# Kernel tuning notes

Measured on AMD Instinct MI355X. Metric: run time of the kernel, lower is better.

## Reference

```python
import jax, jax.numpy as jnp
import numpy as np

B, M, N, C = 8, 4096, 4096, 3


def setup_inputs() -> dict:
    key = jax.random.key(0)
    k1, k2 = jax.random.split(key)
    set1 = jax.random.normal(k1, (B, M, C), dtype=jnp.float32)
    set2 = jax.random.normal(k2, (B, N, C), dtype=jnp.float32)
    return {"set1": set1, "set2": set2}


def _pairwise_dist(set1, set2):
    # ||a - b|| computed via expansion to avoid a (B,M,N,C) broadcast tensor.
    sq1 = jnp.sum(set1 * set1, axis=-1)  # (B, M)
    sq2 = jnp.sum(set2 * set2, axis=-1)  # (B, N)
    inner = jnp.einsum("bmc,bnc->bmn", set1, set2)  # (B, M, N)
    d2 = sq1[:, :, None] + sq2[:, None, :] - 2.0 * inner
    return jnp.sqrt(jnp.maximum(d2, 0.0))  # (B, M, N)


def reference(set1, set2):
    # Average (Chamfer-style) Hausdorff: mean of directed nearest-neighbor
    # distances in both directions, summed.  Output shape (B,).
    d = _pairwise_dist(set1, set2)                # (B, M, N)
    term_1 = jnp.mean(jnp.min(d, axis=2), axis=1)  # set1 -> set2
    term_2 = jnp.mean(jnp.min(d, axis=1), axis=1)  # set2 -> set1
    res = term_1 + term_2
    if res.shape[0] == 1:
        res = jnp.squeeze(res, axis=0)
    return res
```

## Files before the change

kernel.cpp:

```cpp
#include <hip/hip_runtime.h>
#include <hip/hip_bf16.h>
#include <math.h>

constexpr int NB   = 8;
constexpr int NPTS = 4096;
constexpr int NSEG = 4;
constexpr int NN   = NPTS / NSEG;

typedef __attribute__((ext_vector_type(8)))  short  short8;
typedef __attribute__((ext_vector_type(16))) float  f32x16;

__device__ inline unsigned short f2bf(float v) {
    __hip_bfloat16 t = __float2bfloat16(v);
    return *reinterpret_cast<unsigned short*>(&t);
}
__device__ inline float bf2f(unsigned short u) {
    __hip_bfloat16 t = *reinterpret_cast<__hip_bfloat16*>(&u);
    return __bfloat162float(t);
}

__global__ __launch_bounds__(256, 4) void mfma_min_kernel(
    const float* __restrict__ s1, const float* __restrict__ s2,
    float* __restrict__ pmin)
{
    __shared__ short8 blds[2048];

    int bid  = blockIdx.x;
    int nseg = bid & 3;
    int qb   = (bid >> 2) & 15;
    int g    = bid >> 6;
    int b    = g & 7, dir = g >> 3;

    const float* Q    = dir ? s2 : s1;
    const float* Tset = dir ? s1 : s2;

    int tid = threadIdx.x;
    int wid = tid >> 6, l = tid & 63;
    int c = l & 31, h = l >> 5;

    const float* tsrc = Tset + ((size_t)b * NPTS + (size_t)nseg * NN) * 3;
    #pragma unroll
    for (int k = 0; k < 4; ++k) {
        int p = k * 256 + tid;
        float x = tsrc[p*3+0], y = tsrc[p*3+1], z = tsrc[p*3+2];
        float sq = fmaf(z, z, fmaf(y, y, x * x));
        float tx = -2.0f*x, ty = -2.0f*y, tz = -2.0f*z;
        unsigned short thx = f2bf(tx), thy = f2bf(ty), thz = f2bf(tz);
        unsigned short tlx = f2bf(tx - bf2f(thx));
        unsigned short tly = f2bf(ty - bf2f(thy));
        unsigned short tlz = f2bf(tz - bf2f(thz));
        unsigned short sqh = f2bf(sq);
        unsigned short sql = f2bf(sq - bf2f(sqh));
        short8 tLo = {(short)thx,(short)thy,(short)thz,(short)thx,(short)thy,(short)thz,(short)sqh,(short)sql};
        short8 tHi = {(short)tlx,(short)tly,(short)tlz,0,0,0,0,0};
        int slot = (p >> 5) * 64 + (p & 31);
        blds[slot]      = tLo;
        blds[slot + 32] = tHi;
    }

    short8 qfr[2];
    #pragma unroll
    for (int f = 0; f < 2; ++f) {
        int qidx = qb * 256 + wid * 64 + f * 32 + c;
        const float* qp = Q + ((size_t)b * NPTS + qidx) * 3;
        float x = qp[0], y = qp[1], z = qp[2];
        unsigned short ahx = f2bf(x), ahy = f2bf(y), ahz = f2bf(z);
        if (h == 0) {
            unsigned short alx = f2bf(x - bf2f(ahx));
            unsigned short aly = f2bf(y - bf2f(ahy));
            unsigned short alz = f2bf(z - bf2f(ahz));
            unsigned short one = 0x3F80;
            qfr[f] = short8{(short)ahx,(short)ahy,(short)ahz,
                            (short)alx,(short)aly,(short)alz,(short)one,(short)one};
        } else {
            qfr[f] = short8{(short)ahx,(short)ahy,(short)ahz,0,0,0,0,0};
        }
    }
    __syncthreads();

    f32x16 zero, acc0, acc1;
    #pragma unroll
    for (int r = 0; r < 16; ++r) { zero[r] = 0.0f; acc0[r] = 3.4e38f; acc1[r] = 3.4e38f; }

    for (int i = 0; i < 16; ++i) {
        short8 t0 = blds[(2*i  ) * 64 + l];
        short8 t1 = blds[(2*i+1) * 64 + l];
        {
            f32x16 d0 = __builtin_amdgcn_mfma_f32_32x32x16_bf16(t0, qfr[0], zero, 0, 0, 0);
            f32x16 d1 = __builtin_amdgcn_mfma_f32_32x32x16_bf16(t1, qfr[0], zero, 0, 0, 0);
            #pragma unroll
            for (int r = 0; r < 16; ++r)
                acc0[r] = fminf(fminf(acc0[r], d0[r]), d1[r]);
        }
        {
            f32x16 d0 = __builtin_amdgcn_mfma_f32_32x32x16_bf16(t0, qfr[1], zero, 0, 0, 0);
            f32x16 d1 = __builtin_amdgcn_mfma_f32_32x32x16_bf16(t1, qfr[1], zero, 0, 0, 0);
            #pragma unroll
            for (int r = 0; r < 16; ++r)
                acc1[r] = fminf(fminf(acc1[r], d0[r]), d1[r]);
        }
    }

    float* pg = pmin + ((size_t)g * NSEG + nseg) * NPTS;
    #pragma unroll
    for (int f = 0; f < 2; ++f) {
        f32x16& a = f ? acc1 : acc0;
        float v = a[0];
        #pragma unroll
        for (int r = 1; r < 16; ++r) v = fminf(v, a[r]);
        v = fminf(v, __shfl_xor(v, 32, 64));
        if (h == 0)
            pg[qb * 256 + wid * 64 + f * 32 + c] = v;
    }
}

__global__ __launch_bounds__(1024) void reduce_kernel(
    const float* __restrict__ s1, const float* __restrict__ s2,
    const float* __restrict__ pmin, float* __restrict__ out)
{
    int b = blockIdx.x;
    int t = threadIdx.x;

    float sum = 0.0f;
    #pragma unroll
    for (int dir = 0; dir < 2; ++dir) {
        int g = dir * NB + b;
        const float4* pg = reinterpret_cast<const float4*>(pmin + (size_t)g * NSEG * NPTS);
        float4 m = pg[t];
        #pragma unroll
        for (int s = 1; s < NSEG; ++s) {
            float4 v = pg[(size_t)s * 1024 + t];
            m.x = fminf(m.x, v.x); m.y = fminf(m.y, v.y);
            m.z = fminf(m.z, v.z); m.w = fminf(m.w, v.w);
        }
        const float* q = (dir ? s2 : s1) + ((size_t)b * NPTS + (size_t)4 * t) * 3;
        const float4* q4 = reinterpret_cast<const float4*>(q);
        float4 f0 = q4[0], f1 = q4[1], f2 = q4[2];
        float sa0 = fmaf(f0.z, f0.z, fmaf(f0.y, f0.y, f0.x * f0.x));
        float sa1 = fmaf(f1.y, f1.y, fmaf(f1.x, f1.x, f0.w * f0.w));
        float sa2 = fmaf(f2.x, f2.x, fmaf(f1.w, f1.w, f1.z * f1.z));
        float sa3 = fmaf(f2.w, f2.w, fmaf(f2.z, f2.z, f2.y * f2.y));
        sum += sqrtf(fmaxf(sa0 + m.x, 0.0f)) + sqrtf(fmaxf(sa1 + m.y, 0.0f))
             + sqrtf(fmaxf(sa2 + m.z, 0.0f)) + sqrtf(fmaxf(sa3 + m.w, 0.0f));
    }

    for (int off = 32; off > 0; off >>= 1)
        sum += __shfl_down(sum, off, 64);

    __shared__ float red[16];
    if ((t & 63) == 0) red[t >> 6] = sum;
    __syncthreads();
    if (t == 0) {
        float tt = 0.0f;
        #pragma unroll
        for (int w = 0; w < 16; ++w) tt += red[w];
        out[b] = tt * (1.0f / (float)NPTS);
    }
}

extern "C" void kernel_launch(void* const* d_in, const int* in_sizes, int n_in,
                              void* d_out, int out_size, void* d_ws, size_t ws_size,
                              hipStream_t stream) {
    const float* set1 = (const float*)d_in[0];
    const float* set2 = (const float*)d_in[1];
    float* out  = (float*)d_out;
    float* pmin = (float*)d_ws;

    mfma_min_kernel<<<16 * 16 * NSEG, 256, 0, stream>>>(set1, set2, pmin);
    reduce_kernel<<<NB, 1024, 0, stream>>>(set1, set2, pmin, out);
}
```

Before: 18.23 us.

## Fold query norms into min kernel and split reduction across more blocks

The main kernel now adds each query point's squared norm to its partial minimum before storing, so the reduction no longer rereads the input point sets. The single 8-block reduction is replaced by a 64-block partial reduction plus a tiny final kernel that combines the two directions per batch. The aim is more parallelism in the tail reduction, at the cost of an extra kernel launch.

```diff
diff --git a/kernel.cpp b/kernel.cpp
--- a/kernel.cpp
+++ b/kernel.cpp
@@ -58,12 +58,13 @@
         blds[slot + 32] = tHi;
     }
 
-    short8 qfr[2];
+    short8 qfr[2]; float qx[2], qy[2], qz[2];
     #pragma unroll
     for (int f = 0; f < 2; ++f) {
         int qidx = qb * 256 + wid * 64 + f * 32 + c;
         const float* qp = Q + ((size_t)b * NPTS + qidx) * 3;
         float x = qp[0], y = qp[1], z = qp[2];
+        qx[f] = x; qy[f] = y; qz[f] = z;
         unsigned short ahx = f2bf(x), ahy = f2bf(y), ahz = f2bf(z);
         if (h == 0) {
             unsigned short alx = f2bf(x - bf2f(ahx));
@@ -109,53 +110,57 @@
         #pragma unroll
         for (int r = 1; r < 16; ++r) v = fminf(v, a[r]);
         v = fminf(v, __shfl_xor(v, 32, 64));
-        if (h == 0)
-            pg[qb * 256 + wid * 64 + f * 32 + c] = v;
+        if (h == 0) {
+            float sa = fmaf(qz[f], qz[f], fmaf(qy[f], qy[f], qx[f] * qx[f]));
+            pg[qb * 256 + wid * 64 + f * 32 + c] = sa + v;
+        }
     }
 }
 
-__global__ __launch_bounds__(1024) void reduce_kernel(
-    const float* __restrict__ s1, const float* __restrict__ s2,
-    const float* __restrict__ pmin, float* __restrict__ out)
+__global__ __launch_bounds__(256) void reduce_kernel(
+    const float* __restrict__ pmin, float* __restrict__ partial)
 {
-    int b = blockIdx.x;
-    int t = threadIdx.x;
+    int bid = blockIdx.x;
+    int qc  = bid & 3;
+    int g   = bid >> 2;
+    int t   = threadIdx.x;
+    int col = qc * 256 + t;
 
-    float sum = 0.0f;
+    const float4* pg = reinterpret_cast<const float4*>(
+        pmin + (size_t)g * NSEG * NPTS) + col;
+
+    float4 m = pg[0];
     #pragma unroll
-    for (int dir = 0; dir < 2; ++dir) {
-        int g = dir * NB + b;
-        const float4* pg = reinterpret_cast<const float4*>(pmin + (size_t)g * NSEG * NPTS);
-        float4 m = pg[t];
-        #pragma unroll
-        for (int s = 1; s < NSEG; ++s) {
-            float4 v = pg[(size_t)s * 1024 + t];
-            m.x = fminf(m.x, v.x); m.y = fminf(m.y, v.y);
-            m.z = fminf(m.z, v.z); m.w = fminf(m.w, v.w);
-        }
-        const float* q = (dir ? s2 : s1) + ((size_t)b * NPTS + (size_t)4 * t) * 3;
-        const float4* q4 = reinterpret_cast<const float4*>(q);
-        float4 f0 = q4[0], f1 = q4[1], f2 = q4[2];
-        float sa0 = fmaf(f0.z, f0.z, fmaf(f0.y, f0.y, f0.x * f0.x));
-        float sa1 = fmaf(f1.y, f1.y, fmaf(f1.x, f1.x, f0.w * f0.w));
-        float sa2 = fmaf(f2.x, f2.x, fmaf(f1.w, f1.w, f1.z * f1.z));
-        float sa3 = fmaf(f2.w, f2.w, fmaf(f2.z, f2.z, f2.y * f2.y));
-        sum += sqrtf(fmaxf(sa0 + m.x, 0.0f)) + sqrtf(fmaxf(sa1 + m.y, 0.0f))
-             + sqrtf(fmaxf(sa2 + m.z, 0.0f)) + sqrtf(fmaxf(sa3 + m.w, 0.0f));
+    for (int s = 1; s < NSEG; ++s) {
+        float4 v = pg[(size_t)s * 1024];
+        m.x = fminf(m.x, v.x); m.y = fminf(m.y, v.y);
+        m.z = fminf(m.z, v.z); m.w = fminf(m.w, v.w);
     }
+    float sum = sqrtf(fmaxf(m.x, 0.0f)) + sqrtf(fmaxf(m.y, 0.0f))
+              + sqrtf(fmaxf(m.z, 0.0f)) + sqrtf(fmaxf(m.w, 0.0f));
 
     for (int off = 32; off > 0; off >>= 1)
         sum += __shfl_down(sum, off, 64);
 
-    __shared__ float red[16];
+    __shared__ float red[4];
     if ((t & 63) == 0) red[t >> 6] = sum;
     __syncthreads();
-    if (t == 0) {
-        float tt = 0.0f;
+    if (t == 0) partial[bid] = red[0] + red[1] + red[2] + red[3];
+}
+
+__global__ __launch_bounds__(64) void final_kernel(
+    const float* __restrict__ partial, float* __restrict__ out)
+{
+    int l = threadIdx.x;
+    float s = 0.0f;
+    if (l < 16) {
         #pragma unroll
-        for (int w = 0; w < 16; ++w) tt += red[w];
-        out[b] = tt * (1.0f / (float)NPTS);
+        for (int j = 0; j < 4; ++j)
+            s += partial[l * 4 + j];
     }
+    float other = __shfl(s, l + 8, 64);
+    if (l < NB)
+        out[l] = (s + other) * (1.0f / (float)NPTS);
 }
 
 extern "C" void kernel_launch(void* const* d_in, const int* in_sizes, int n_in,
@@ -163,9 +168,11 @@
                               hipStream_t stream) {
     const float* set1 = (const float*)d_in[0];
     const float* set2 = (const float*)d_in[1];
-    float* out  = (float*)d_out;
-    float* pmin = (float*)d_ws;
+    float* out     = (float*)d_out;
+    float* pmin    = (float*)d_ws;
+    float* partial = pmin + (size_t)2 * NB * NSEG * NPTS;
 
     mfma_min_kernel<<<16 * 16 * NSEG, 256, 0, stream>>>(set1, set2, pmin);
-    reduce_kernel<<<NB, 1024, 0, stream>>>(set1, set2, pmin, out);
+    reduce_kernel<<<16 * 4, 256, 0, stream>>>(pmin, partial);
+    final_kernel<<<1, 64, 0, stream>>>(partial, out);
 }
```

Result: no change. 18.20 us (-0.1%).
